# Kernel tuning notes

Hardware: AMD Instinct MI355X
Metric: run time of the kernel (lower is better)

Reference implementation:

```python
import jax, jax.numpy as jnp
import numpy as np

# ---- constants from the module ----
E_L, E_e, E_i = -65.0, 0.0, -80.0
V_th, V_reset, V_floor = -50.0, -65.0, -200.0
dt = 0.25
T_STEPS = 4000
DECAY_AMPA = float(np.exp(-dt / 2.0))   # tau_ampa = 2.0
DECAY_GABA = float(np.exp(-dt / 9.0))   # tau_gaba = 9.0
C_M_E, G_L_E = 1.0, 1.0 / 20.0          # tau_m_E = 20
C_M_I, G_L_I = 0.5, 0.5 / 5.0           # tau_m_I = 5
REF_E = 12                               # round(3.0/0.25)
REF_I = 6                                # round(1.5/0.25)
CM_BACK = 80.0
SLOPE = 1.0                              # biophysical surrogate slope

@jax.custom_vjp
def spike(u):
    # Heaviside forward, fast-sigmoid surrogate backward (SurrogateSpike)
    return (u >= 0).astype(u.dtype)

def _spike_fwd(u):
    return (u >= 0).astype(u.dtype), u

def _spike_bwd(u, g):
    return (g * SLOPE / (1.0 + SLOPE * jnp.abs(u)) ** 2,)

spike.defvjp(_spike_fwd, _spike_bwd)

def _scale_grad(x, scale):
    # forward identity, gradient scaled by `scale`
    return x * scale + jax.lax.stop_gradient(x) * (1.0 - scale)

def lif_step(v, I_total, ref, C_m, g_L, ref_steps):
    dv = (dt / C_m) * (-g_L * (v - E_L) + I_total)
    dv = _scale_grad(dv, 1.0 / CM_BACK)
    v = jnp.maximum(v + dv, V_floor)
    ref = jnp.maximum(ref - 1, 0)
    can_spike = ref == 0
    s = spike(v - V_th) * can_spike.astype(v.dtype)
    spiked_or_ref = (s > 0) | ~can_spike
    v = jnp.where(spiked_or_ref, V_reset, v)
    ref = jnp.where(s > 0, ref_steps, ref)
    return v, s, ref

def setup_inputs() -> dict:
    key = jax.random.key(0)
    ks = jax.random.split(key, 6)
    T, B, N_IN, N_E, N_I, N_OUT = T_STEPS, 64, 64, 256, 64, 10

    def init_w(k, shape, mean, std):
        # init_weight: N(mean,std) clamped >=0, fan-in normalized
        w = jnp.maximum(jax.random.normal(k, shape, jnp.float32) * std + mean, 0.0)
        return w / shape[0]

    return {
        "input_spikes": (jax.random.uniform(ks[0], (T, B, N_IN)) < 0.02).astype(jnp.float32),
        "W_ff0": init_w(ks[1], (N_IN, N_E), 5.1, 3.8),
        "W_ff1": init_w(ks[2], (N_E, N_OUT), 5.1, 3.8),
        "W_ee": init_w(ks[3], (N_E, N_E), 0.0, 0.0),
        "W_ei": init_w(ks[4], (N_E, N_I), 1.0, 0.5),
        "W_ie": init_w(ks[5], (N_I, N_E), 3.0, 1.5),
    }

def reference(input_spikes, W_ff0, W_ff1, W_ee, W_ei, W_ie):
    # Dale's law: feedforward weights clamped >= 0 in forward
    W0 = jnp.maximum(W_ff0, 0.0)
    W1 = jnp.maximum(W_ff1, 0.0)
    B = input_spikes.shape[1]
    N_E, N_I, N_OUT = W0.shape[1], W_ei.shape[1], W1.shape[1]
    f32 = input_spikes.dtype

    z = lambda n: jnp.zeros((B, n), f32)
    vl = lambda n: jnp.full((B, n), E_L, f32)
    zr = lambda n: jnp.zeros((B, n), jnp.int32)

    carry0 = (vl(N_E), zr(N_E), z(N_E), z(N_E), z(N_E),   # E pop: v, ref, g_ampa, g_gaba, spikes
              vl(N_I), zr(N_I), z(N_I), z(N_I),           # I pop: v, ref, g_ampa, spikes
              vl(N_OUT), zr(N_OUT), z(N_OUT),             # out pop: v, ref, g_ampa
              z(N_OUT))                                    # output spike accumulator

    def step(c, s_in):
        v_e, r_e, ge_e, gi_e, s_e, v_i, r_i, ge_i, s_i, v_o, r_o, g_o, acc = c
        # exp_synapse: spike kicks first, then decay
        ge_e = (ge_e + s_in @ W0 + s_e @ W_ee) * DECAY_AMPA
        gi_e = (gi_e + s_i @ W_ie) * DECAY_GABA
        ge_i = (ge_i + s_e @ W_ei) * DECAY_AMPA
        # E neurons: COBA with excitation + inhibition
        v_e, s_e, r_e = lif_step(v_e, ge_e * (E_e - v_e) + gi_e * (E_i - v_e), r_e, C_M_E, G_L_E, REF_E)
        # I neurons: COBA excitation only
        v_i, s_i, r_i = lif_step(v_i, ge_i * (E_e - v_i), r_i, C_M_I, G_L_I, REF_I)
        # output layer driven by fresh E spikes
        g_o = (g_o + s_e @ W1) * DECAY_AMPA
        v_o, s_o, r_o = lif_step(v_o, g_o * (E_e - v_o), r_o, C_M_E, G_L_E, REF_E)
        acc = acc + s_o
        return (v_e, r_e, ge_e, gi_e, s_e, v_i, r_i, ge_i, s_i, v_o, r_o, g_o, acc), None

    cT, _ = jax.lax.scan(step, carry0, input_spikes)
    return cT[-1]  # [B, N_OUT] output spike counts over T_steps
```

## Files before the change

### kernel.cpp

```cpp
#include <hip/hip_runtime.h>
#include <math.h>

#pragma clang fp contract(off)

#define BB 64
#define N_IN 64
#define N_E 256
#define N_I 64
#define N_OUT 10

__device__ inline unsigned long long rfl64(unsigned long long x) {
  unsigned int lo = __builtin_amdgcn_readfirstlane((unsigned int)x);
  unsigned int hi = __builtin_amdgcn_readfirstlane((unsigned int)(x >> 32));
  return (((unsigned long long)hi) << 32) | (unsigned long long)lo;
}

__global__ __launch_bounds__(256, 1) void ping_kernel(
    const float* __restrict__ g_in,
    const float* __restrict__ g_W0,
    const float* __restrict__ g_W1,
    const float* __restrict__ g_Wee,
    const float* __restrict__ g_Wei,
    const float* __restrict__ g_Wie,
    float* __restrict__ g_out,
    int T, float dA, float dG)
{
  const int tid  = threadIdx.x;
  const int lane = tid & 63;
  const int wav  = tid >> 6;
  const int b    = blockIdx.x;
  const int col  = (lane < N_OUT) ? lane : 0;
  const int colO = 64 + col;

  __shared__ float sWie[N_I * N_E];
  __shared__ float sWeiO[N_E * 80];
  __shared__ float sZeroRow[256];
  __shared__ __align__(16) float sPK[2][64][4];
  __shared__ __align__(16) float sKoT[2][16][4];
  __shared__ __align__(16) unsigned sTag[2][4];
  __shared__ unsigned long long sME[2][4];
  __shared__ int sWee;

  {
    const float4* s0 = (const float4*)g_Wie; float4* d0 = (float4*)sWie;
    for (int k = tid; k < (N_I * N_E) / 4; k += 256) d0[k] = s0[k];
    {
      int j = tid;
      float* row = &sWeiO[j * 80];
      for (int c = 0; c < 64; ++c) row[c] = g_Wei[j * N_I + c];
      for (int o = 0; o < N_OUT; ++o) row[64 + o] = fmaxf(g_W1[j * N_OUT + o], 0.f);
      for (int c = 74; c < 80; ++c) row[c] = 0.f;
    }
  }
  sZeroRow[tid] = 0.f;
  if (tid < 4) { sME[0][tid] = 0ull; sME[1][tid] = 0ull; }
  if (tid < 8) sTag[tid >> 2][tid & 3] = 0u;
  if (tid == 0) sWee = 0;
  {
    bool any = false;
    const float4* p = (const float4*)g_Wee;
    for (int k = tid; k < (N_E * N_E) / 4; k += 256) {
      float4 x = p[k];
      any |= (x.x != 0.f) | (x.y != 0.f) | (x.z != 0.f) | (x.w != 0.f);
    }
    if (__ballot(any) != 0ull && lane == 0) sWee = 1;
  }
  __syncthreads();
  const int wee = sWee;

  float vE = -65.f, ge = 0.f, gi = 0.f; int rE = 0;
  float vI = -65.f, gI = 0.f; int rI = 0;
  float vO = -65.f, gO = 0.f, accO = 0.f; int rO = 0;

  unsigned long long mE = 0ull;
  unsigned long long mI = 0ull;

  float cur = g_in[b * N_IN + lane];
  float n1  = g_in[((T > 1 ? 1 : 0) * BB + b) * N_IN + lane];

  unsigned long long mInC = __ballot(cur != 0.f);
  unsigned long long aRemC = 0ull;
  bool vaC[4] = {false, false, false, false};
  float fwC[4];
  if (mInC) {
    unsigned long long a = mInC;
    int ja[4];
#pragma unroll
    for (int k = 0; k < 4; ++k) {
      vaC[k] = (a != 0ull); ja[k] = vaC[k] ? (__ffsll(a) - 1) : 0; a &= (a - 1ull);
    }
    aRemC = a;
#pragma unroll
    for (int k = 0; k < 4; ++k) fwC[k] = g_W0[ja[k] * N_E + tid];
  }

  const int base64 = wav * 64;

  if (!wee) {
    for (int t = 0; t < T; ++t) {
      const int slot = t & 1;
      const int tp = (t + 2 < T) ? (t + 2) : (T - 1);
      float n2 = g_in[(tp * BB + b) * N_IN + lane];

      float pEI = 0.f, kow = 0.f;
      {
        unsigned long long e = mE;
        while (e) {
          const float* qb[4];
#pragma unroll
          for (int k = 0; k < 4; ++k) {
            bool v = (e != 0ull); int j = v ? (__ffsll(e) - 1) : 0; e &= (e - 1ull);
            qb[k] = v ? &sWeiO[(base64 + j) * 80] : sZeroRow;
          }
          float fq[4], fr[4];
#pragma unroll
          for (int k = 0; k < 4; ++k) { fq[k] = qb[k][lane]; fr[k] = qb[k][colO]; }
#pragma unroll
          for (int k = 0; k < 4; ++k) pEI += fq[k];
#pragma unroll
          for (int k = 0; k < 4; ++k) kow += fr[k];
        }
      }

      sPK[slot][lane][wav] = pEI;
      if (lane < 16) sKoT[slot][lane][wav] = kow;
      asm volatile("" ::: "memory");
      if (lane == 0) *((volatile unsigned*)&sTag[slot][wav]) = (unsigned)(t + 1);

      unsigned long long pr0 = ((volatile unsigned long long*)&sTag[slot][0])[0];
      unsigned long long pr1 = ((volatile unsigned long long*)&sTag[slot][0])[1];

      float kie = 0.f;
      {
        unsigned long long c = mI;
        while (c) {
          const float* pb[8];
#pragma unroll
          for (int k = 0; k < 8; ++k) {
            bool v = (c != 0ull); int j = v ? (__ffsll(c) - 1) : 0; c &= (c - 1ull);
            pb[k] = v ? &sWie[j * N_E] : sZeroRow;
          }
          float fI[8];
#pragma unroll
          for (int k = 0; k < 8; ++k) fI[k] = pb[k][tid];
#pragma unroll
          for (int k = 0; k < 8; ++k) kie += fI[k];
        }
      }

      float kin = 0.f;
      if (mInC) {
#pragma unroll
        for (int k = 0; k < 4; ++k) kin += vaC[k] ? fmaxf(fwC[k], 0.f) : 0.f;
        while (aRemC) {
          int j = __ffsll(aRemC) - 1; aRemC &= (aRemC - 1ull);
          kin += fmaxf(g_W0[j * N_E + tid], 0.f);
        }
      }

      ge = (ge + kin) * dA;
      gi = (gi + kie) * dG;
      {
        float t2 = ge * (0.f - vE);
        float t3 = gi * (-80.f - vE);
        float Itot = t2 + t3;
        float dv = 0.25f * ((-0.05f) * (vE - (-65.f)) + Itot);
        dv = dv * 0.0125f + dv * 0.9875f;
        vE = fmaxf(vE + dv, -200.f);
        rE = rE - 1; if (rE < 0) rE = 0;
        bool can = (rE == 0);
        bool sE = ((vE - (-50.f)) >= 0.f) && can;
        vE = (sE || !can) ? -65.f : vE;
        rE = sE ? 12 : rE;
        mE = __ballot(sE);
      }

      mInC = __ballot(n1 != 0.f);
      aRemC = 0ull;
      vaC[0] = vaC[1] = vaC[2] = vaC[3] = false;
      if (mInC) {
        unsigned long long a = mInC;
        int ja[4];
#pragma unroll
        for (int k = 0; k < 4; ++k) {
          vaC[k] = (a != 0ull); ja[k] = vaC[k] ? (__ffsll(a) - 1) : 0; a &= (a - 1ull);
        }
        aRemC = a;
#pragma unroll
        for (int k = 0; k < 4; ++k) fwC[k] = g_W0[ja[k] * N_E + tid];
      }

      {
        const unsigned want = (unsigned)(t + 1);
        const unsigned long long want2 = (((unsigned long long)want) << 32) | want;
        if ((((pr0 ^ want2) | (pr1 ^ want2))) != 0ull) {
          volatile unsigned long long* vt = (volatile unsigned long long*)&sTag[slot][0];
          while (true) {
            unsigned long long a0 = vt[0], a1 = vt[1];
            if (((a0 ^ want2) | (a1 ^ want2)) == 0ull) break;
          }
        }
        asm volatile("" ::: "memory");
      }

      float4 P = *(const float4*)&sPK[slot][lane][0];
      float4 K = *(const float4*)&sKoT[slot][col][0];

      {
        float p = ((P.x + P.y) + P.z) + P.w;
        gI = (gI + p) * dA;
        float Ii = gI * (0.f - vI);
        float dvi = 0.5f * ((-0.1f) * (vI - (-65.f)) + Ii);
        dvi = dvi * 0.0125f + dvi * 0.9875f;
        vI = fmaxf(vI + dvi, -200.f);
        rI = rI - 1; if (rI < 0) rI = 0;
        bool canI = (rI == 0);
        bool sI = ((vI - (-50.f)) >= 0.f) && canI;
        vI = (sI || !canI) ? -65.f : vI;
        rI = sI ? 6 : rI;
        mI = __ballot(sI);
      }

      {
        float ko = ((K.x + K.y) + K.z) + K.w;
        gO = (gO + ko) * dA;
        float Io = gO * (0.f - vO);
        float dvo = 0.25f * ((-0.05f) * (vO - (-65.f)) + Io);
        dvo = dvo * 0.0125f + dvo * 0.9875f;
        vO = fmaxf(vO + dvo, -200.f);
        rO = rO - 1; if (rO < 0) rO = 0;
        bool canO = (rO == 0);
        bool sO = ((vO - (-50.f)) >= 0.f) && canO;
        vO = (sO || !canO) ? -65.f : vO;
        rO = sO ? 12 : rO;
        accO += sO ? 1.f : 0.f;
      }

      cur = n1; n1 = n2;
    }
  } else {
    unsigned long long we0 = 0ull, we1 = 0ull, we2 = 0ull, we3 = 0ull;
    for (int t = 0; t < T; ++t) {
      const int slot = t & 1;
      const int tp = (t + 2 < T) ? (t + 2) : (T - 1);
      float n2 = g_in[(tp * BB + b) * N_IN + lane];

      float pEI = 0.f, kow = 0.f;
      {
        unsigned long long e = mE;
        while (e) {
          const float* qb[4];
#pragma unroll
          for (int k = 0; k < 4; ++k) {
            bool v = (e != 0ull); int j = v ? (__ffsll(e) - 1) : 0; e &= (e - 1ull);
            qb[k] = v ? &sWeiO[(base64 + j) * 80] : sZeroRow;
          }
          float fq[4], fr[4];
#pragma unroll
          for (int k = 0; k < 4; ++k) { fq[k] = qb[k][lane]; fr[k] = qb[k][colO]; }
#pragma unroll
          for (int k = 0; k < 4; ++k) pEI += fq[k];
#pragma unroll
          for (int k = 0; k < 4; ++k) kow += fr[k];
        }
      }
      sPK[slot][lane][wav] = pEI;
      if (lane < 16) sKoT[slot][lane][wav] = kow;
      asm volatile("s_waitcnt lgkmcnt(0)" ::: "memory");
      if (lane == 0) *((volatile unsigned*)&sTag[slot][wav]) = (unsigned)(t + 1);

      float kie = 0.f;
      {
        unsigned long long c = mI;
        while (c) {
          const float* pb[8];
#pragma unroll
          for (int k = 0; k < 8; ++k) {
            bool v = (c != 0ull); int j = v ? (__ffsll(c) - 1) : 0; c &= (c - 1ull);
            pb[k] = v ? &sWie[j * N_E] : sZeroRow;
          }
          float fI[8];
#pragma unroll
          for (int k = 0; k < 8; ++k) fI[k] = pb[k][tid];
#pragma unroll
          for (int k = 0; k < 8; ++k) kie += fI[k];
        }
      }

      float kin = 0.f;
      if (mInC) {
#pragma unroll
        for (int k = 0; k < 4; ++k) kin += vaC[k] ? fmaxf(fwC[k], 0.f) : 0.f;
        while (aRemC) {
          int j = __ffsll(aRemC) - 1; aRemC &= (aRemC - 1ull);
          kin += fmaxf(g_W0[j * N_E + tid], 0.f);
        }
      }

      float kee = 0.f;
      {
        unsigned long long m0 = we0, m1 = we1, m2 = we2, m3 = we3;
        while (m0 | m1 | m2 | m3) {
          bool h0 = (m0 != 0ull), h1 = (m1 != 0ull), h2 = (m2 != 0ull), h3 = (m3 != 0ull);
          int idx = 0;
          if (h0)      { idx = __ffsll(m0) - 1;       m0 &= (m0 - 1ull); }
          else if (h1) { idx = 64 + __ffsll(m1) - 1;  m1 &= (m1 - 1ull); }
          else if (h2) { idx = 128 + __ffsll(m2) - 1; m2 &= (m2 - 1ull); }
          else if (h3) { idx = 192 + __ffsll(m3) - 1; m3 &= (m3 - 1ull); }
          kee += g_Wee[idx * N_E + tid];
        }
      }

      ge = ((ge + kin) + kee) * dA;
      gi = (gi + kie) * dG;
      {
        float t2 = ge * (0.f - vE);
        float t3 = gi * (-80.f - vE);
        float Itot = t2 + t3;
        float dv = 0.25f * ((-0.05f) * (vE - (-65.f)) + Itot);
        dv = dv * 0.0125f + dv * 0.9875f;
        vE = fmaxf(vE + dv, -200.f);
        rE = rE - 1; if (rE < 0) rE = 0;
        bool can = (rE == 0);
        bool sE = ((vE - (-50.f)) >= 0.f) && can;
        vE = (sE || !can) ? -65.f : vE;
        rE = sE ? 12 : rE;
        unsigned long long fresh = __ballot(sE);
        if (lane == 0) sME[slot][wav] = fresh;
        mE = fresh;
      }

      mInC = __ballot(n1 != 0.f);
      aRemC = 0ull;
      vaC[0] = vaC[1] = vaC[2] = vaC[3] = false;
      if (mInC) {
        unsigned long long a = mInC;
        int ja[4];
#pragma unroll
        for (int k = 0; k < 4; ++k) {
          vaC[k] = (a != 0ull); ja[k] = vaC[k] ? (__ffsll(a) - 1) : 0; a &= (a - 1ull);
        }
        aRemC = a;
#pragma unroll
        for (int k = 0; k < 4; ++k) fwC[k] = g_W0[ja[k] * N_E + tid];
      }

      {
        const unsigned want = (unsigned)(t + 1);
        const unsigned long long want2 = (((unsigned long long)want) << 32) | want;
        volatile unsigned long long* vt = (volatile unsigned long long*)&sTag[slot][0];
        while (true) {
          unsigned long long a0 = vt[0], a1 = vt[1];
          if (((a0 ^ want2) | (a1 ^ want2)) == 0ull) break;
        }
        asm volatile("" ::: "memory");
      }

      float4 P = *(const float4*)&sPK[slot][lane][0];
      float4 K = *(const float4*)&sKoT[slot][col][0];

      {
        float p = ((P.x + P.y) + P.z) + P.w;
        gI = (gI + p) * dA;
        float Ii = gI * (0.f - vI);
        float dvi = 0.5f * ((-0.1f) * (vI - (-65.f)) + Ii);
        dvi = dvi * 0.0125f + dvi * 0.9875f;
        vI = fmaxf(vI + dvi, -200.f);
        rI = rI - 1; if (rI < 0) rI = 0;
        bool canI = (rI == 0);
        bool sI = ((vI - (-50.f)) >= 0.f) && canI;
        vI = (sI || !canI) ? -65.f : vI;
        rI = sI ? 6 : rI;
        mI = __ballot(sI);
      }

      {
        float ko = ((K.x + K.y) + K.z) + K.w;
        gO = (gO + ko) * dA;
        float Io = gO * (0.f - vO);
        float dvo = 0.25f * ((-0.05f) * (vO - (-65.f)) + Io);
        dvo = dvo * 0.0125f + dvo * 0.9875f;
        vO = fmaxf(vO + dvo, -200.f);
        rO = rO - 1; if (rO < 0) rO = 0;
        bool canO = (rO == 0);
        bool sO = ((vO - (-50.f)) >= 0.f) && canO;
        vO = (sO || !canO) ? -65.f : vO;
        rO = sO ? 12 : rO;
        accO += sO ? 1.f : 0.f;
      }

      __syncthreads();
      we0 = rfl64(sME[slot][0]); we1 = rfl64(sME[slot][1]);
      we2 = rfl64(sME[slot][2]); we3 = rfl64(sME[slot][3]);

      cur = n1; n1 = n2;
    }
  }

  {
    float kd = 0.f;
    unsigned long long e = mE;
    while (e) {
      const float* rb[4];
#pragma unroll
      for (int k = 0; k < 4; ++k) {
        bool v = (e != 0ull); int j = v ? (__ffsll(e) - 1) : 0; e &= (e - 1ull);
        rb[k] = v ? &sWeiO[(base64 + j) * 80] : sZeroRow;
      }
      float fr[4];
#pragma unroll
      for (int k = 0; k < 4; ++k) fr[k] = rb[k][colO];
#pragma unroll
      for (int k = 0; k < 4; ++k) kd += fr[k];
    }
    __syncthreads();
    if (lane < 16) sKoT[0][lane][wav] = kd;
    __syncthreads();
    float4 K = *(const float4*)&sKoT[0][col][0];
    float ko = ((K.x + K.y) + K.z) + K.w;
    gO = (gO + ko) * dA;
    float Io = gO * (0.f - vO);
    float dvo = 0.25f * ((-0.05f) * (vO - (-65.f)) + Io);
    dvo = dvo * 0.0125f + dvo * 0.9875f;
    vO = fmaxf(vO + dvo, -200.f);
    rO = rO - 1; if (rO < 0) rO = 0;
    bool canO = (rO == 0);
    bool sO = ((vO - (-50.f)) >= 0.f) && canO;
    accO += sO ? 1.f : 0.f;
  }

  if (wav == 0 && lane < N_OUT) g_out[b * N_OUT + lane] = accO;
}

extern "C" void kernel_launch(void* const* d_in, const int* in_sizes, int n_in,
                              void* d_out, int out_size, void* d_ws, size_t ws_size,
                              hipStream_t stream) {
  const float* g_in  = (const float*)d_in[0];
  const float* g_W0  = (const float*)d_in[1];
  const float* g_W1  = (const float*)d_in[2];
  const float* g_Wee = (const float*)d_in[3];
  const float* g_Wei = (const float*)d_in[4];
  const float* g_Wie = (const float*)d_in[5];
  float* out = (float*)d_out;
  int T = in_sizes[0] / (BB * N_IN);
  float dA = (float)exp(-0.25 / 2.0);
  float dG = (float)exp(-0.25 / 9.0);
  ping_kernel<<<dim3(BB), dim3(256), 0, stream>>>(g_in, g_W0, g_W1, g_Wee, g_Wei, g_Wie, out, T, dA, dG);
}
```

Measured before the change: 4.770 ms.

## Collapse block to single wavefront handling four E neurons per lane, removing inter-wave sync

The kernel now launches one 64-lane wavefront per batch row instead of four waves. Each lane owns four E neurons, so the per-step cross-wave exchange through shared memory (tag spin-waits and __syncthreads) is gone. W_ie is transposed in LDS so each lane reads a float4 per inhibitory spike, and the wee and no-wee paths are merged. The cost is four times the serial E-side work per lane and less latency hiding, in exchange for removing barrier and spin-wait overhead on a latency-bound recurrence.

After: 8.366 ms. +75.4%, slower.

```diff
diff --git a/kernel.cpp b/kernel.cpp
--- a/kernel.cpp
+++ b/kernel.cpp
@@ -9,13 +9,7 @@
 #define N_I 64
 #define N_OUT 10
 
-__device__ inline unsigned long long rfl64(unsigned long long x) {
-  unsigned int lo = __builtin_amdgcn_readfirstlane((unsigned int)x);
-  unsigned int hi = __builtin_amdgcn_readfirstlane((unsigned int)(x >> 32));
-  return (((unsigned long long)hi) << 32) | (unsigned long long)lo;
-}
-
-__global__ __launch_bounds__(256, 1) void ping_kernel(
+__global__ __launch_bounds__(64, 1) void ping_kernel(
     const float* __restrict__ g_in,
     const float* __restrict__ g_W0,
     const float* __restrict__ g_W1,
@@ -25,54 +19,60 @@
     float* __restrict__ g_out,
     int T, float dA, float dG)
 {
-  const int tid  = threadIdx.x;
-  const int lane = tid & 63;
-  const int wav  = tid >> 6;
+  const int lane = threadIdx.x;
   const int b    = blockIdx.x;
   const int col  = (lane < N_OUT) ? lane : 0;
   const int colO = 64 + col;
 
-  __shared__ float sWie[N_I * N_E];
-  __shared__ float sWeiO[N_E * 80];
-  __shared__ float sZeroRow[256];
-  __shared__ __align__(16) float sPK[2][64][4];
-  __shared__ __align__(16) float sKoT[2][16][4];
-  __shared__ __align__(16) unsigned sTag[2][4];
-  __shared__ unsigned long long sME[2][4];
-  __shared__ int sWee;
+  __shared__ __align__(16) float sWieT[N_I * 64 * 4];
+  __shared__ __align__(16) float sWeiO[N_E * 80];
+  __shared__ __align__(16) float sZeroRow[256];
 
   {
-    const float4* s0 = (const float4*)g_Wie; float4* d0 = (float4*)sWie;
-    for (int k = tid; k < (N_I * N_E) / 4; k += 256) d0[k] = s0[k];
-    {
-      int j = tid;
-      float* row = &sWeiO[j * 80];
-      for (int c = 0; c < 64; ++c) row[c] = g_Wei[j * N_I + c];
-      for (int o = 0; o < N_OUT; ++o) row[64 + o] = fmaxf(g_W1[j * N_OUT + o], 0.f);
-      for (int c = 74; c < 80; ++c) row[c] = 0.f;
-    }
-  }
-  sZeroRow[tid] = 0.f;
-  if (tid < 4) { sME[0][tid] = 0ull; sME[1][tid] = 0ull; }
-  if (tid < 8) sTag[tid >> 2][tid & 3] = 0u;
-  if (tid == 0) sWee = 0;
+    const float4* wie4 = (const float4*)g_Wie;
+    for (int k = lane; k < 64 * 64; k += 64) {
+      int j = k >> 6, c4 = k & 63;
+      float4 v = wie4[k];
+      int e0 = 4 * c4;
+      sWieT[(j * 64 + ((e0 + 0) & 63)) * 4 + ((e0 + 0) >> 6)] = v.x;
+      sWieT[(j * 64 + ((e0 + 1) & 63)) * 4 + ((e0 + 1) >> 6)] = v.y;
+      sWieT[(j * 64 + ((e0 + 2) & 63)) * 4 + ((e0 + 2) >> 6)] = v.z;
+      sWieT[(j * 64 + ((e0 + 3) & 63)) * 4 + ((e0 + 3) >> 6)] = v.w;
+    }
+    const float4* wei4 = (const float4*)g_Wei;
+    for (int k = lane; k < 256 * 16; k += 64) {
+      int r = k >> 4, c4 = k & 15;
+      *(float4*)&sWeiO[r * 80 + c4 * 4] = wei4[k];
+    }
+    for (int k = lane; k < 256 * N_OUT; k += 64) {
+      int r = k / N_OUT, o = k - r * N_OUT;
+      sWeiO[r * 80 + 64 + o] = fmaxf(g_W1[k], 0.f);
+    }
+    for (int k = lane; k < 256 * 6; k += 64) {
+      int r = k / 6, c = k - r * 6;
+      sWeiO[r * 80 + 74 + c] = 0.f;
+    }
+    for (int k = lane; k < 256; k += 64) sZeroRow[k] = 0.f;
+  }
+  bool wee;
   {
     bool any = false;
     const float4* p = (const float4*)g_Wee;
-    for (int k = tid; k < (N_E * N_E) / 4; k += 256) {
+    for (int k = lane; k < (N_E * N_E) / 4; k += 64) {
       float4 x = p[k];
       any |= (x.x != 0.f) | (x.y != 0.f) | (x.z != 0.f) | (x.w != 0.f);
     }
-    if (__ballot(any) != 0ull && lane == 0) sWee = 1;
+    wee = (__ballot(any) != 0ull);
   }
   __syncthreads();
-  const int wee = sWee;
-
-  float vE = -65.f, ge = 0.f, gi = 0.f; int rE = 0;
+
+  float vE[4], ge[4], gi[4]; int rE[4];
+#pragma unroll
+  for (int g = 0; g < 4; ++g) { vE[g] = -65.f; ge[g] = 0.f; gi[g] = 0.f; rE[g] = 0; }
   float vI = -65.f, gI = 0.f; int rI = 0;
   float vO = -65.f, gO = 0.f, accO = 0.f; int rO = 0;
 
-  unsigned long long mE = 0ull;
+  unsigned long long mEw[4] = {0ull, 0ull, 0ull, 0ull};
   unsigned long long mI = 0ull;
 
   float cur = g_in[b * N_IN + lane];
@@ -81,7 +81,7 @@
   unsigned long long mInC = __ballot(cur != 0.f);
   unsigned long long aRemC = 0ull;
   bool vaC[4] = {false, false, false, false};
-  float fwC[4];
+  float fw[4][4];
   if (mInC) {
     unsigned long long a = mInC;
     int ja[4];
@@ -91,333 +91,180 @@
     }
     aRemC = a;
 #pragma unroll
-    for (int k = 0; k < 4; ++k) fwC[k] = g_W0[ja[k] * N_E + tid];
-  }
-
-  const int base64 = wav * 64;
-
-  if (!wee) {
-    for (int t = 0; t < T; ++t) {
-      const int slot = t & 1;
-      const int tp = (t + 2 < T) ? (t + 2) : (T - 1);
-      float n2 = g_in[(tp * BB + b) * N_IN + lane];
-
-      float pEI = 0.f, kow = 0.f;
-      {
-        unsigned long long e = mE;
-        while (e) {
-          const float* qb[4];
-#pragma unroll
-          for (int k = 0; k < 4; ++k) {
-            bool v = (e != 0ull); int j = v ? (__ffsll(e) - 1) : 0; e &= (e - 1ull);
-            qb[k] = v ? &sWeiO[(base64 + j) * 80] : sZeroRow;
-          }
-          float fq[4], fr[4];
-#pragma unroll
-          for (int k = 0; k < 4; ++k) { fq[k] = qb[k][lane]; fr[k] = qb[k][colO]; }
-#pragma unroll
-          for (int k = 0; k < 4; ++k) pEI += fq[k];
-#pragma unroll
-          for (int k = 0; k < 4; ++k) kow += fr[k];
-        }
-      }
-
-      sPK[slot][lane][wav] = pEI;
-      if (lane < 16) sKoT[slot][lane][wav] = kow;
-      asm volatile("" ::: "memory");
-      if (lane == 0) *((volatile unsigned*)&sTag[slot][wav]) = (unsigned)(t + 1);
-
-      unsigned long long pr0 = ((volatile unsigned long long*)&sTag[slot][0])[0];
-      unsigned long long pr1 = ((volatile unsigned long long*)&sTag[slot][0])[1];
-
-      float kie = 0.f;
-      {
-        unsigned long long c = mI;
-        while (c) {
-          const float* pb[8];
-#pragma unroll
-          for (int k = 0; k < 8; ++k) {
-            bool v = (c != 0ull); int j = v ? (__ffsll(c) - 1) : 0; c &= (c - 1ull);
-            pb[k] = v ? &sWie[j * N_E] : sZeroRow;
-          }
-          float fI[8];
-#pragma unroll
-          for (int k = 0; k < 8; ++k) fI[k] = pb[k][tid];
-#pragma unroll
-          for (int k = 0; k < 8; ++k) kie += fI[k];
-        }
-      }
-
-      float kin = 0.f;
-      if (mInC) {
-#pragma unroll
-        for (int k = 0; k < 4; ++k) kin += vaC[k] ? fmaxf(fwC[k], 0.f) : 0.f;
-        while (aRemC) {
-          int j = __ffsll(aRemC) - 1; aRemC &= (aRemC - 1ull);
-          kin += fmaxf(g_W0[j * N_E + tid], 0.f);
-        }
-      }
-
-      ge = (ge + kin) * dA;
-      gi = (gi + kie) * dG;
-      {
-        float t2 = ge * (0.f - vE);
-        float t3 = gi * (-80.f - vE);
-        float Itot = t2 + t3;
-        float dv = 0.25f * ((-0.05f) * (vE - (-65.f)) + Itot);
-        dv = dv * 0.0125f + dv * 0.9875f;
-        vE = fmaxf(vE + dv, -200.f);
-        rE = rE - 1; if (rE < 0) rE = 0;
-        bool can = (rE == 0);
-        bool sE = ((vE - (-50.f)) >= 0.f) && can;
-        vE = (sE || !can) ? -65.f : vE;
-        rE = sE ? 12 : rE;
-        mE = __ballot(sE);
-      }
-
-      mInC = __ballot(n1 != 0.f);
-      aRemC = 0ull;
-      vaC[0] = vaC[1] = vaC[2] = vaC[3] = false;
-      if (mInC) {
-        unsigned long long a = mInC;
-        int ja[4];
-#pragma unroll
-        for (int k = 0; k < 4; ++k) {
-          vaC[k] = (a != 0ull); ja[k] = vaC[k] ? (__ffsll(a) - 1) : 0; a &= (a - 1ull);
-        }
-        aRemC = a;
-#pragma unroll
-        for (int k = 0; k < 4; ++k) fwC[k] = g_W0[ja[k] * N_E + tid];
-      }
-
-      {
-        const unsigned want = (unsigned)(t + 1);
-        const unsigned long long want2 = (((unsigned long long)want) << 32) | want;
-        if ((((pr0 ^ want2) | (pr1 ^ want2))) != 0ull) {
-          volatile unsigned long long* vt = (volatile unsigned long long*)&sTag[slot][0];
-          while (true) {
-            unsigned long long a0 = vt[0], a1 = vt[1];
-            if (((a0 ^ want2) | (a1 ^ want2)) == 0ull) break;
-          }
-        }
-        asm volatile("" ::: "memory");
-      }
-
-      float4 P = *(const float4*)&sPK[slot][lane][0];
-      float4 K = *(const float4*)&sKoT[slot][col][0];
-
-      {
-        float p = ((P.x + P.y) + P.z) + P.w;
-        gI = (gI + p) * dA;
-        float Ii = gI * (0.f - vI);
-        float dvi = 0.5f * ((-0.1f) * (vI - (-65.f)) + Ii);
-        dvi = dvi * 0.0125f + dvi * 0.9875f;
-        vI = fmaxf(vI + dvi, -200.f);
-        rI = rI - 1; if (rI < 0) rI = 0;
-        bool canI = (rI == 0);
-        bool sI = ((vI - (-50.f)) >= 0.f) && canI;
-        vI = (sI || !canI) ? -65.f : vI;
-        rI = sI ? 6 : rI;
-        mI = __ballot(sI);
-      }
-
-      {
-        float ko = ((K.x + K.y) + K.z) + K.w;
-        gO = (gO + ko) * dA;
-        float Io = gO * (0.f - vO);
-        float dvo = 0.25f * ((-0.05f) * (vO - (-65.f)) + Io);
-        dvo = dvo * 0.0125f + dvo * 0.9875f;
-        vO = fmaxf(vO + dvo, -200.f);
-        rO = rO - 1; if (rO < 0) rO = 0;
-        bool canO = (rO == 0);
-        bool sO = ((vO - (-50.f)) >= 0.f) && canO;
-        vO = (sO || !canO) ? -65.f : vO;
-        rO = sO ? 12 : rO;
-        accO += sO ? 1.f : 0.f;
-      }
-
-      cur = n1; n1 = n2;
-    }
-  } else {
-    unsigned long long we0 = 0ull, we1 = 0ull, we2 = 0ull, we3 = 0ull;
-    for (int t = 0; t < T; ++t) {
-      const int slot = t & 1;
-      const int tp = (t + 2 < T) ? (t + 2) : (T - 1);
-      float n2 = g_in[(tp * BB + b) * N_IN + lane];
-
-      float pEI = 0.f, kow = 0.f;
-      {
-        unsigned long long e = mE;
-        while (e) {
-          const float* qb[4];
-#pragma unroll
-          for (int k = 0; k < 4; ++k) {
-            bool v = (e != 0ull); int j = v ? (__ffsll(e) - 1) : 0; e &= (e - 1ull);
-            qb[k] = v ? &sWeiO[(base64 + j) * 80] : sZeroRow;
-          }
-          float fq[4], fr[4];
-#pragma unroll
-          for (int k = 0; k < 4; ++k) { fq[k] = qb[k][lane]; fr[k] = qb[k][colO]; }
-#pragma unroll
-          for (int k = 0; k < 4; ++k) pEI += fq[k];
-#pragma unroll
-          for (int k = 0; k < 4; ++k) kow += fr[k];
-        }
-      }
-      sPK[slot][lane][wav] = pEI;
-      if (lane < 16) sKoT[slot][lane][wav] = kow;
-      asm volatile("s_waitcnt lgkmcnt(0)" ::: "memory");
-      if (lane == 0) *((volatile unsigned*)&sTag[slot][wav]) = (unsigned)(t + 1);
-
-      float kie = 0.f;
-      {
-        unsigned long long c = mI;
-        while (c) {
-          const float* pb[8];
-#pragma unroll
-          for (int k = 0; k < 8; ++k) {
-            bool v = (c != 0ull); int j = v ? (__ffsll(c) - 1) : 0; c &= (c - 1ull);
-            pb[k] = v ? &sWie[j * N_E] : sZeroRow;
-          }
-          float fI[8];
-#pragma unroll
-          for (int k = 0; k < 8; ++k) fI[k] = pb[k][tid];
-#pragma unroll
-          for (int k = 0; k < 8; ++k) kie += fI[k];
-        }
-      }
-
-      float kin = 0.f;
-      if (mInC) {
-#pragma unroll
-        for (int k = 0; k < 4; ++k) kin += vaC[k] ? fmaxf(fwC[k], 0.f) : 0.f;
-        while (aRemC) {
-          int j = __ffsll(aRemC) - 1; aRemC &= (aRemC - 1ull);
-          kin += fmaxf(g_W0[j * N_E + tid], 0.f);
-        }
-      }
-
-      float kee = 0.f;
-      {
-        unsigned long long m0 = we0, m1 = we1, m2 = we2, m3 = we3;
-        while (m0 | m1 | m2 | m3) {
-          bool h0 = (m0 != 0ull), h1 = (m1 != 0ull), h2 = (m2 != 0ull), h3 = (m3 != 0ull);
-          int idx = 0;
-          if (h0)      { idx = __ffsll(m0) - 1;       m0 &= (m0 - 1ull); }
-          else if (h1) { idx = 64 + __ffsll(m1) - 1;  m1 &= (m1 - 1ull); }
-          else if (h2) { idx = 128 + __ffsll(m2) - 1; m2 &= (m2 - 1ull); }
-          else if (h3) { idx = 192 + __ffsll(m3) - 1; m3 &= (m3 - 1ull); }
-          kee += g_Wee[idx * N_E + tid];
-        }
-      }
-
-      ge = ((ge + kin) + kee) * dA;
-      gi = (gi + kie) * dG;
-      {
-        float t2 = ge * (0.f - vE);
-        float t3 = gi * (-80.f - vE);
-        float Itot = t2 + t3;
-        float dv = 0.25f * ((-0.05f) * (vE - (-65.f)) + Itot);
-        dv = dv * 0.0125f + dv * 0.9875f;
-        vE = fmaxf(vE + dv, -200.f);
-        rE = rE - 1; if (rE < 0) rE = 0;
-        bool can = (rE == 0);
-        bool sE = ((vE - (-50.f)) >= 0.f) && can;
-        vE = (sE || !can) ? -65.f : vE;
-        rE = sE ? 12 : rE;
-        unsigned long long fresh = __ballot(sE);
-        if (lane == 0) sME[slot][wav] = fresh;
-        mE = fresh;
-      }
-
-      mInC = __ballot(n1 != 0.f);
-      aRemC = 0ull;
-      vaC[0] = vaC[1] = vaC[2] = vaC[3] = false;
-      if (mInC) {
-        unsigned long long a = mInC;
-        int ja[4];
-#pragma unroll
-        for (int k = 0; k < 4; ++k) {
-          vaC[k] = (a != 0ull); ja[k] = vaC[k] ? (__ffsll(a) - 1) : 0; a &= (a - 1ull);
-        }
-        aRemC = a;
-#pragma unroll
-        for (int k = 0; k < 4; ++k) fwC[k] = g_W0[ja[k] * N_E + tid];
-      }
-
-      {
-        const unsigned want = (unsigned)(t + 1);
-        const unsigned long long want2 = (((unsigned long long)want) << 32) | want;
-        volatile unsigned long long* vt = (volatile unsigned long long*)&sTag[slot][0];
-        while (true) {
-          unsigned long long a0 = vt[0], a1 = vt[1];
-          if (((a0 ^ want2) | (a1 ^ want2)) == 0ull) break;
-        }
-        asm volatile("" ::: "memory");
-      }
-
-      float4 P = *(const float4*)&sPK[slot][lane][0];
-      float4 K = *(const float4*)&sKoT[slot][col][0];
-
-      {
-        float p = ((P.x + P.y) + P.z) + P.w;
-        gI = (gI + p) * dA;
-        float Ii = gI * (0.f - vI);
-        float dvi = 0.5f * ((-0.1f) * (vI - (-65.f)) + Ii);
-        dvi = dvi * 0.0125f + dvi * 0.9875f;
-        vI = fmaxf(vI + dvi, -200.f);
-        rI = rI - 1; if (rI < 0) rI = 0;
-        bool canI = (rI == 0);
-        bool sI = ((vI - (-50.f)) >= 0.f) && canI;
-        vI = (sI || !canI) ? -65.f : vI;
-        rI = sI ? 6 : rI;
-        mI = __ballot(sI);
-      }
-
-      {
-        float ko = ((K.x + K.y) + K.z) + K.w;
-        gO = (gO + ko) * dA;
-        float Io = gO * (0.f - vO);
-        float dvo = 0.25f * ((-0.05f) * (vO - (-65.f)) + Io);
-        dvo = dvo * 0.0125f + dvo * 0.9875f;
-        vO = fmaxf(vO + dvo, -200.f);
-        rO = rO - 1; if (rO < 0) rO = 0;
-        bool canO = (rO == 0);
-        bool sO = ((vO - (-50.f)) >= 0.f) && canO;
-        vO = (sO || !canO) ? -65.f : vO;
-        rO = sO ? 12 : rO;
-        accO += sO ? 1.f : 0.f;
-      }
-
-      __syncthreads();
-      we0 = rfl64(sME[slot][0]); we1 = rfl64(sME[slot][1]);
-      we2 = rfl64(sME[slot][2]); we3 = rfl64(sME[slot][3]);
-
-      cur = n1; n1 = n2;
-    }
+    for (int k = 0; k < 4; ++k)
+#pragma unroll
+      for (int g = 0; g < 4; ++g)
+        fw[k][g] = g_W0[ja[k] * N_E + lane + 64 * g];
+  }
+
+  for (int t = 0; t < T; ++t) {
+    const int tp = (t + 2 < T) ? (t + 2) : (T - 1);
+    float n2 = g_in[(tp * BB + b) * N_IN + lane];
+
+    float pEI[4], kow[4];
+#pragma unroll
+    for (int g = 0; g < 4; ++g) {
+      float p = 0.f, ko = 0.f;
+      unsigned long long e = mEw[g];
+      while (e) {
+        const float* qb[8];
+#pragma unroll
+        for (int k = 0; k < 8; ++k) {
+          bool v = (e != 0ull); int j = v ? (__ffsll(e) - 1) : 0; e &= (e - 1ull);
+          qb[k] = v ? &sWeiO[(g * 64 + j) * 80] : sZeroRow;
+        }
+        float fq[8], fr[8];
+#pragma unroll
+        for (int k = 0; k < 8; ++k) { fq[k] = qb[k][lane]; fr[k] = qb[k][colO]; }
+#pragma unroll
+        for (int k = 0; k < 8; ++k) p += fq[k];
+#pragma unroll
+        for (int k = 0; k < 8; ++k) ko += fr[k];
+      }
+      pEI[g] = p; kow[g] = ko;
+    }
+
+    float kie[4] = {0.f, 0.f, 0.f, 0.f};
+    {
+      unsigned long long c = mI;
+      while (c) {
+        const float* pb[8];
+#pragma unroll
+        for (int k = 0; k < 8; ++k) {
+          bool v = (c != 0ull); int j = v ? (__ffsll(c) - 1) : 0; c &= (c - 1ull);
+          pb[k] = v ? &sWieT[j * 256] : sZeroRow;
+        }
+        float4 f[8];
+#pragma unroll
+        for (int k = 0; k < 8; ++k) f[k] = *(const float4*)&pb[k][lane * 4];
+#pragma unroll
+        for (int k = 0; k < 8; ++k) {
+          kie[0] += f[k].x; kie[1] += f[k].y; kie[2] += f[k].z; kie[3] += f[k].w;
+        }
+      }
+    }
+
+    float kin[4] = {0.f, 0.f, 0.f, 0.f};
+    if (mInC) {
+#pragma unroll
+      for (int k = 0; k < 4; ++k)
+#pragma unroll
+        for (int g = 0; g < 4; ++g)
+          kin[g] += vaC[k] ? fmaxf(fw[k][g], 0.f) : 0.f;
+      while (aRemC) {
+        int j = __ffsll(aRemC) - 1; aRemC &= (aRemC - 1ull);
+#pragma unroll
+        for (int g = 0; g < 4; ++g)
+          kin[g] += fmaxf(g_W0[j * N_E + lane + 64 * g], 0.f);
+      }
+    }
+
+    float kee[4] = {0.f, 0.f, 0.f, 0.f};
+    if (wee) {
+      unsigned long long m0 = mEw[0], m1 = mEw[1], m2 = mEw[2], m3 = mEw[3];
+      while (m0 | m1 | m2 | m3) {
+        int idx = 0;
+        if (m0)      { idx = __ffsll(m0) - 1;       m0 &= (m0 - 1ull); }
+        else if (m1) { idx = 64 + __ffsll(m1) - 1;  m1 &= (m1 - 1ull); }
+        else if (m2) { idx = 128 + __ffsll(m2) - 1; m2 &= (m2 - 1ull); }
+        else         { idx = 192 + __ffsll(m3) - 1; m3 &= (m3 - 1ull); }
+#pragma unroll
+        for (int g = 0; g < 4; ++g)
+          kee[g] += g_Wee[idx * N_E + lane + 64 * g];
+      }
+    }
+
+#pragma unroll
+    for (int g = 0; g < 4; ++g) {
+      ge[g] = ((ge[g] + kin[g]) + kee[g]) * dA;
+      gi[g] = (gi[g] + kie[g]) * dG;
+      float t2 = ge[g] * (0.f - vE[g]);
+      float t3 = gi[g] * (-80.f - vE[g]);
+      float Itot = t2 + t3;
+      float dv = 0.25f * ((-0.05f) * (vE[g] - (-65.f)) + Itot);
+      dv = dv * 0.0125f + dv * 0.9875f;
+      vE[g] = fmaxf(vE[g] + dv, -200.f);
+      rE[g] = rE[g] - 1; if (rE[g] < 0) rE[g] = 0;
+      bool can = (rE[g] == 0);
+      bool sE = ((vE[g] - (-50.f)) >= 0.f) && can;
+      vE[g] = (sE || !can) ? -65.f : vE[g];
+      rE[g] = sE ? 12 : rE[g];
+      mEw[g] = __ballot(sE);
+    }
+
+    mInC = __ballot(n1 != 0.f);
+    aRemC = 0ull;
+    vaC[0] = vaC[1] = vaC[2] = vaC[3] = false;
+    if (mInC) {
+      unsigned long long a = mInC;
+      int ja[4];
+#pragma unroll
+      for (int k = 0; k < 4; ++k) {
+        vaC[k] = (a != 0ull); ja[k] = vaC[k] ? (__ffsll(a) - 1) : 0; a &= (a - 1ull);
+      }
+      aRemC = a;
+#pragma unroll
+      for (int k = 0; k < 4; ++k)
+#pragma unroll
+        for (int g = 0; g < 4; ++g)
+          fw[k][g] = g_W0[ja[k] * N_E + lane + 64 * g];
+    }
+
+    {
+      float p = ((pEI[0] + pEI[1]) + pEI[2]) + pEI[3];
+      gI = (gI + p) * dA;
+      float Ii = gI * (0.f - vI);
+      float dvi = 0.5f * ((-0.1f) * (vI - (-65.f)) + Ii);
+      dvi = dvi * 0.0125f + dvi * 0.9875f;
+      vI = fmaxf(vI + dvi, -200.f);
+      rI = rI - 1; if (rI < 0) rI = 0;
+      bool canI = (rI == 0);
+      bool sI = ((vI - (-50.f)) >= 0.f) && canI;
+      vI = (sI || !canI) ? -65.f : vI;
+      rI = sI ? 6 : rI;
+      mI = __ballot(sI);
+    }
+
+    {
+      float ko = ((kow[0] + kow[1]) + kow[2]) + kow[3];
+      gO = (gO + ko) * dA;
+      float Io = gO * (0.f - vO);
+      float dvo = 0.25f * ((-0.05f) * (vO - (-65.f)) + Io);
+      dvo = dvo * 0.0125f + dvo * 0.9875f;
+      vO = fmaxf(vO + dvo, -200.f);
+      rO = rO - 1; if (rO < 0) rO = 0;
+      bool canO = (rO == 0);
+      bool sO = ((vO - (-50.f)) >= 0.f) && canO;
+      vO = (sO || !canO) ? -65.f : vO;
+      rO = sO ? 12 : rO;
+      accO += sO ? 1.f : 0.f;
+    }
+
+    cur = n1; n1 = n2;
   }
 
   {
-    float kd = 0.f;
-    unsigned long long e = mE;
-    while (e) {
-      const float* rb[4];
-#pragma unroll
-      for (int k = 0; k < 4; ++k) {
-        bool v = (e != 0ull); int j = v ? (__ffsll(e) - 1) : 0; e &= (e - 1ull);
-        rb[k] = v ? &sWeiO[(base64 + j) * 80] : sZeroRow;
-      }
-      float fr[4];
-#pragma unroll
-      for (int k = 0; k < 4; ++k) fr[k] = rb[k][colO];
-#pragma unroll
-      for (int k = 0; k < 4; ++k) kd += fr[k];
-    }
-    __syncthreads();
-    if (lane < 16) sKoT[0][lane][wav] = kd;
-    __syncthreads();
-    float4 K = *(const float4*)&sKoT[0][col][0];
-    float ko = ((K.x + K.y) + K.z) + K.w;
+    float kd[4];
+#pragma unroll
+    for (int g = 0; g < 4; ++g) {
+      float k2 = 0.f;
+      unsigned long long e = mEw[g];
+      while (e) {
+        const float* rb[8];
+#pragma unroll
+        for (int k = 0; k < 8; ++k) {
+          bool v = (e != 0ull); int j = v ? (__ffsll(e) - 1) : 0; e &= (e - 1ull);
+          rb[k] = v ? &sWeiO[(g * 64 + j) * 80] : sZeroRow;
+        }
+        float fr[8];
+#pragma unroll
+        for (int k = 0; k < 8; ++k) fr[k] = rb[k][colO];
+#pragma unroll
+        for (int k = 0; k < 8; ++k) k2 += fr[k];
+      }
+      kd[g] = k2;
+    }
+    float ko = ((kd[0] + kd[1]) + kd[2]) + kd[3];
     gO = (gO + ko) * dA;
     float Io = gO * (0.f - vO);
     float dvo = 0.25f * ((-0.05f) * (vO - (-65.f)) + Io);
@@ -429,7 +276,7 @@
     accO += sO ? 1.f : 0.f;
   }
 
-  if (wav == 0 && lane < N_OUT) g_out[b * N_OUT + lane] = accO;
+  if (lane < N_OUT) g_out[b * N_OUT + lane] = accO;
 }
 
 extern "C" void kernel_launch(void* const* d_in, const int* in_sizes, int n_in,
@@ -445,5 +292,5 @@
   int T = in_sizes[0] / (BB * N_IN);
   float dA = (float)exp(-0.25 / 2.0);
   float dG = (float)exp(-0.25 / 9.0);
-  ping_kernel<<<dim3(BB), dim3(256), 0, stream>>>(g_in, g_W0, g_W1, g_Wee, g_Wei, g_Wie, out, T, dA, dG);
+  ping_kernel<<<dim3(BB), dim3(64), 0, stream>>>(g_in, g_W0, g_W1, g_Wee, g_Wei, g_Wie, out, T, dA, dG);
 }
```
